# Kernel optimization log

Hardware: AMD Instinct MI355X
Metric: run time of the kernel (lower is better)

Reference implementation:

```python
import jax, jax.numpy as jnp
import numpy as np

B = 524288       # batch
N_QUBITS = 16    # data dimension == wires
LAYERS = 8
N_READOUT = 2    # PauliZ on wires (0, 1)


def setup_inputs() -> dict:
    key = jax.random.key(0)
    k1, k2, k3 = jax.random.split(key, 3)
    X = jax.random.uniform(k1, (B, N_QUBITS), dtype=jnp.float32)
    params = 0.01 * jax.random.normal(k2, (LAYERS, N_QUBITS, 3), dtype=jnp.float32)
    head_w = jax.random.normal(k3, (1, N_READOUT), dtype=jnp.float32) / jnp.sqrt(float(N_READOUT))
    head_b = jnp.zeros((1,), dtype=jnp.float32)
    return {"X": X, "params": params, "head_w": head_w, "head_b": head_b}


def _rot_matrix(phi, theta, omega):
    """PennyLane qml.Rot(phi, theta, omega) = RZ(omega) RY(theta) RZ(phi); [Q,2,2] complex."""
    ct = jnp.cos(theta * 0.5)
    st = jnp.sin(theta * 0.5)
    m00 = jnp.exp(-0.5j * (phi + omega)) * ct
    m01 = -jnp.exp(0.5j * (phi - omega)) * st
    m10 = jnp.exp(-0.5j * (phi - omega)) * st
    m11 = jnp.exp(0.5j * (phi + omega)) * ct
    return jnp.stack([jnp.stack([m00, m01], axis=-1),
                      jnp.stack([m10, m11], axis=-1)], axis=-2)


def reference(X, params, head_w, head_b):
    # No entanglement (default) -> circuit is a product of single-qubit circuits;
    # simulate per-(batch, qubit) 2-amplitude states, fully batched.
    half = X * 0.5
    # AngleEmbedding (RX per wire) applied to |0>: (cos(x/2), -i sin(x/2))
    state = jnp.stack([jnp.cos(half) + 0j, -1j * jnp.sin(half)], axis=-1)  # [B,Q,2] c64
    for l in range(params.shape[0]):
        M = _rot_matrix(params[l, :, 0], params[l, :, 1], params[l, :, 2])  # [Q,2,2]
        state = jnp.einsum('qij,bqj->bqi', M, state)
    probs = state.real ** 2 + state.imag ** 2            # [B,Q,2]
    ez = probs[..., 0] - probs[..., 1]                   # <Z> per wire, [B,Q]
    E = ez[:, :N_READOUT]                                # readout wires (0, 1)
    logits = E @ head_w.T + head_b                       # [B,1]
    return logits.squeeze(-1)
```

## Files before the change

kernel.cpp:

```cpp
#include <hip/hip_runtime.h>
#include <math.h>

#define NQ 16
#define LAYERS 8

struct M22 {
    float r00, i00, r01, i01, r10, i10, r11, i11;
};

__device__ __forceinline__ M22 cmul(const M22& A, const M22& B) {
    M22 p;
    p.r00 = A.r00*B.r00 - A.i00*B.i00 + A.r01*B.r10 - A.i01*B.i10;
    p.i00 = A.r00*B.i00 + A.i00*B.r00 + A.r01*B.i10 + A.i01*B.r10;
    p.r01 = A.r00*B.r01 - A.i00*B.i01 + A.r01*B.r11 - A.i01*B.i11;
    p.i01 = A.r00*B.i01 + A.i00*B.r01 + A.r01*B.i11 + A.i01*B.r11;
    p.r10 = A.r10*B.r00 - A.i10*B.i00 + A.r11*B.r10 - A.i11*B.i10;
    p.i10 = A.r10*B.i00 + A.i10*B.r00 + A.r11*B.i10 + A.i11*B.r10;
    p.r11 = A.r10*B.r01 - A.i10*B.i01 + A.r11*B.r11 - A.i11*B.i11;
    p.i11 = A.r10*B.i01 + A.i10*B.r01 + A.r11*B.i11 + A.i11*B.r11;
    return p;
}

__device__ __forceinline__ M22 mshfl_xor(const M22& A, int mask) {
    M22 p;
    p.r00 = __shfl_xor(A.r00, mask); p.i00 = __shfl_xor(A.i00, mask);
    p.r01 = __shfl_xor(A.r01, mask); p.i01 = __shfl_xor(A.i01, mask);
    p.r10 = __shfl_xor(A.r10, mask); p.i10 = __shfl_xor(A.i10, mask);
    p.r11 = __shfl_xor(A.r11, mask); p.i11 = __shfl_xor(A.i11, mask);
    return p;
}

__global__ __launch_bounds__(256) void vqc_fused(
        const float* __restrict__ X,
        const float* __restrict__ params,
        const float* __restrict__ head_w,
        const float* __restrict__ head_b,
        float* __restrict__ out,
        int n)
{
    __shared__ float sC[6];

    int tid = threadIdx.x;
    int b = blockIdx.x * blockDim.x + tid;

    float2 x = make_float2(0.f, 0.f);
    if (b < n) x = *(const float2*)(X + (size_t)b * NQ);

    if (tid < 16) {
        int q = tid >> 3;
        int l = tid & 7;
        float phi = params[(l * NQ + q) * 3 + 0];
        float th  = params[(l * NQ + q) * 3 + 1];
        float om  = params[(l * NQ + q) * 3 + 2];
        float ct, st, c_p, s_p, c_m, s_m;
        __sincosf(0.5f * th, &st, &ct);
        __sincosf(-0.5f * (phi + om), &s_p, &c_p);
        __sincosf( 0.5f * (phi - om), &s_m, &c_m);
        M22 U;
        U.r00 =  c_p * ct;  U.i00 =  s_p * ct;
        U.r01 = -c_m * st;  U.i01 = -s_m * st;
        U.r10 =  c_m * st;  U.i10 = -s_m * st;
        U.r11 =  c_p * ct;  U.i11 = -s_p * ct;

        #pragma unroll
        for (int mask = 1; mask <= 4; mask <<= 1) {
            M22 other = mshfl_xor(U, mask);
            bool upper = (tid & mask) != 0;
            M22 left  = upper ? U : other;
            M22 right = upper ? other : U;
            U = cmul(left, right);
        }

        if (l == 0) {
            float d0 = (U.r00*U.r00 + U.i00*U.i00) - (U.r10*U.r10 + U.i10*U.i10);
            float d1 = (U.r01*U.r01 + U.i01*U.i01) - (U.r11*U.r11 + U.i11*U.i11);
            float A  = 0.5f * (d0 + d1);
            float Bc = 0.5f * (d0 - d1);
            float im0 = U.i00*U.r01 - U.r00*U.i01;
            float im1 = U.i10*U.r11 - U.r10*U.i11;
            float Bs = -(im0 - im1);
            float w = head_w[q];
            sC[3*q + 0] = w * A;
            sC[3*q + 1] = w * Bc;
            sC[3*q + 2] = w * Bs;
        }
    }
    __syncthreads();

    if (b >= n) return;
    float C  = head_b[0] + sC[0] + sC[3];
    float K0 = sC[1], K1 = sC[2], K2 = sC[4], K3 = sC[5];
    float s0, c0, s1, c1;
    __sincosf(x.x, &s0, &c0);
    __sincosf(x.y, &s1, &c1);
    out[b] = C + K0 * c0 + K1 * s0 + K2 * c1 + K3 * s1;
}

extern "C" void kernel_launch(void* const* d_in, const int* in_sizes, int n_in,
                              void* d_out, int out_size, void* d_ws, size_t ws_size,
                              hipStream_t stream) {
    const float* X      = (const float*)d_in[0];
    const float* params = (const float*)d_in[1];
    const float* head_w = (const float*)d_in[2];
    const float* head_b = (const float*)d_in[3];
    float* out = (float*)d_out;

    int threads = 256;
    int blocks  = (out_size + threads - 1) / threads;
    vqc_fused<<<blocks, threads, 0, stream>>>(X, params, head_w, head_b, out, out_size);
}
```

Measured before the change: 77.69 us.

## Compute circuit coefficients per wavefront via shuffles and process four rows per thread

Removes the shared-memory staging and block-wide barrier by having every wavefront redundantly build the composed rotation unitaries with lane shuffles and broadcast the readout coefficients with __shfl. Each thread now handles four batch rows, issuing four strided float2 loads and one float4 store, with a quarter as many blocks. This cuts barrier and launch overhead and amortizes the parameter setup, at the cost of redundant trig work in every lane and fewer threads to hide the strided-load latency.

```diff
diff --git a/kernel.cpp b/kernel.cpp
--- a/kernel.cpp
+++ b/kernel.cpp
@@ -38,62 +38,83 @@
         float* __restrict__ out,
         int n)
 {
-    __shared__ float sC[6];
+    const int tid  = threadIdx.x;
+    const int lane = tid & 63;
+    const int base = (blockIdx.x * blockDim.x + tid) << 2;
 
-    int tid = threadIdx.x;
-    int b = blockIdx.x * blockDim.x + tid;
+    const float2* X2 = (const float2*)X;
+    float2 x0 = make_float2(0.f, 0.f), x1 = x0, x2 = x0, x3 = x0;
+    if (base + 3 < n) {
+        x0 = X2[(size_t)(base + 0) * 8];
+        x1 = X2[(size_t)(base + 1) * 8];
+        x2 = X2[(size_t)(base + 2) * 8];
+        x3 = X2[(size_t)(base + 3) * 8];
+    } else if (base < n) {
+        x0 = X2[(size_t)base * 8];
+        if (base + 1 < n) x1 = X2[(size_t)(base + 1) * 8];
+        if (base + 2 < n) x2 = X2[(size_t)(base + 2) * 8];
+    }
 
-    float2 x = make_float2(0.f, 0.f);
-    if (b < n) x = *(const float2*)(X + (size_t)b * NQ);
+    const int q = (lane >> 3) & 1;
+    const int l = lane & 7;
+    float phi = params[(l * NQ + q) * 3 + 0];
+    float th  = params[(l * NQ + q) * 3 + 1];
+    float om  = params[(l * NQ + q) * 3 + 2];
+    float ct, st, c_p, s_p, c_m, s_m;
+    __sincosf(0.5f * th, &st, &ct);
+    __sincosf(-0.5f * (phi + om), &s_p, &c_p);
+    __sincosf( 0.5f * (phi - om), &s_m, &c_m);
+    M22 U;
+    U.r00 =  c_p * ct;  U.i00 =  s_p * ct;
+    U.r01 = -c_m * st;  U.i01 = -s_m * st;
+    U.r10 =  c_m * st;  U.i10 = -s_m * st;
+    U.r11 =  c_p * ct;  U.i11 = -s_p * ct;
 
-    if (tid < 16) {
-        int q = tid >> 3;
-        int l = tid & 7;
-        float phi = params[(l * NQ + q) * 3 + 0];
-        float th  = params[(l * NQ + q) * 3 + 1];
-        float om  = params[(l * NQ + q) * 3 + 2];
-        float ct, st, c_p, s_p, c_m, s_m;
-        __sincosf(0.5f * th, &st, &ct);
-        __sincosf(-0.5f * (phi + om), &s_p, &c_p);
-        __sincosf( 0.5f * (phi - om), &s_m, &c_m);
-        M22 U;
-        U.r00 =  c_p * ct;  U.i00 =  s_p * ct;
-        U.r01 = -c_m * st;  U.i01 = -s_m * st;
-        U.r10 =  c_m * st;  U.i10 = -s_m * st;
-        U.r11 =  c_p * ct;  U.i11 = -s_p * ct;
+    #pragma unroll
+    for (int mask = 1; mask <= 4; mask <<= 1) {
+        M22 other = mshfl_xor(U, mask);
+        bool upper = (lane & mask) != 0;
+        M22 left  = upper ? U : other;
+        M22 right = upper ? other : U;
+        U = cmul(left, right);
+    }
 
-        #pragma unroll
-        for (int mask = 1; mask <= 4; mask <<= 1) {
-            M22 other = mshfl_xor(U, mask);
-            bool upper = (tid & mask) != 0;
-            M22 left  = upper ? U : other;
-            M22 right = upper ? other : U;
-            U = cmul(left, right);
-        }
+    float d0 = (U.r00*U.r00 + U.i00*U.i00) - (U.r10*U.r10 + U.i10*U.i10);
+    float d1 = (U.r01*U.r01 + U.i01*U.i01) - (U.r11*U.r11 + U.i11*U.i11);
+    float A  = 0.5f * (d0 + d1);
+    float Bc = 0.5f * (d0 - d1);
+    float im0 = U.i00*U.r01 - U.r00*U.i01;
+    float im1 = U.i10*U.r11 - U.r10*U.i11;
+    float Bs = -(im0 - im1);
+    float w  = head_w[q];
+    float wA = w * A, wBc = w * Bc, wBs = w * Bs;
 
-        if (l == 0) {
-            float d0 = (U.r00*U.r00 + U.i00*U.i00) - (U.r10*U.r10 + U.i10*U.i10);
-            float d1 = (U.r01*U.r01 + U.i01*U.i01) - (U.r11*U.r11 + U.i11*U.i11);
-            float A  = 0.5f * (d0 + d1);
-            float Bc = 0.5f * (d0 - d1);
-            float im0 = U.i00*U.r01 - U.r00*U.i01;
-            float im1 = U.i10*U.r11 - U.r10*U.i11;
-            float Bs = -(im0 - im1);
-            float w = head_w[q];
-            sC[3*q + 0] = w * A;
-            sC[3*q + 1] = w * Bc;
-            sC[3*q + 2] = w * Bs;
-        }
+    const float C  = head_b[0] + __shfl(wA, 0) + __shfl(wA, 8);
+    const float K0 = __shfl(wBc, 0);
+    const float K1 = __shfl(wBs, 0);
+    const float K2 = __shfl(wBc, 8);
+    const float K3 = __shfl(wBs, 8);
+
+    if (base >= n) return;
+
+    float s0, c0, s1, c1;
+    float4 r;
+    __sincosf(x0.x, &s0, &c0); __sincosf(x0.y, &s1, &c1);
+    r.x = C + K0 * c0 + K1 * s0 + K2 * c1 + K3 * s1;
+    __sincosf(x1.x, &s0, &c0); __sincosf(x1.y, &s1, &c1);
+    r.y = C + K0 * c0 + K1 * s0 + K2 * c1 + K3 * s1;
+    __sincosf(x2.x, &s0, &c0); __sincosf(x2.y, &s1, &c1);
+    r.z = C + K0 * c0 + K1 * s0 + K2 * c1 + K3 * s1;
+    __sincosf(x3.x, &s0, &c0); __sincosf(x3.y, &s1, &c1);
+    r.w = C + K0 * c0 + K1 * s0 + K2 * c1 + K3 * s1;
+
+    if (base + 3 < n) {
+        *(float4*)(out + base) = r;
+    } else {
+        out[base] = r.x;
+        if (base + 1 < n) out[base + 1] = r.y;
+        if (base + 2 < n) out[base + 2] = r.z;
     }
-    __syncthreads();
-
-    if (b >= n) return;
-    float C  = head_b[0] + sC[0] + sC[3];
-    float K0 = sC[1], K1 = sC[2], K2 = sC[4], K3 = sC[5];
-    float s0, c0, s1, c1;
-    __sincosf(x.x, &s0, &c0);
-    __sincosf(x.y, &s1, &c1);
-    out[b] = C + K0 * c0 + K1 * s0 + K2 * c1 + K3 * s1;
 }
 
 extern "C" void kernel_launch(void* const* d_in, const int* in_sizes, int n_in,
@@ -106,6 +127,7 @@
     float* out = (float*)d_out;
 
     int threads = 256;
-    int blocks  = (out_size + threads - 1) / threads;
+    int rows_per_block = threads * 4;
+    int blocks = (out_size + rows_per_block - 1) / rows_per_block;
     vqc_fused<<<blocks, threads, 0, stream>>>(X, params, head_w, head_b, out, out_size);
 }
```

Measured after the change: 78.30 us. About the same (+0.8%).
